# Kernel optimization log

Measured on AMD Instinct MI355X. Metric: run time of the kernel, lower is better.

The kernel has to match this reference:

```python
import jax, jax.numpy as jnp
import numpy as np

B, N, T = 4, 512, 10
F = N + 4            # 4 base features + one per-column feature
MSG_HID, MSG_DIM = 128, 32
UPD_HID, OUT_DIM = 128, 4


def setup_inputs() -> dict:
    key = jax.random.key(0)
    ks = jax.random.split(key, 9)
    s = 0.05
    return {
        "x": jax.random.normal(ks[0], (B, N, T, F), dtype=jnp.float32),
        # message MLP: (T*5) -> MSG_HID -> MSG_DIM
        "mW1": jax.random.normal(ks[1], (T * 5, MSG_HID), dtype=jnp.float32) * s,
        "mb1": jnp.zeros((MSG_HID,), dtype=jnp.float32),
        "mW2": jax.random.normal(ks[2], (MSG_HID, MSG_DIM), dtype=jnp.float32) * s,
        "mb2": jnp.zeros((MSG_DIM,), dtype=jnp.float32),
        # update MLP: (MSG_DIM+4) -> UPD_HID -> OUT_DIM
        "iW1": jax.random.normal(ks[3], (MSG_DIM + 4, UPD_HID), dtype=jnp.float32) * s,
        "ib1": jnp.zeros((UPD_HID,), dtype=jnp.float32),
        "iW2": jax.random.normal(ks[4], (UPD_HID, OUT_DIM), dtype=jnp.float32) * s,
        "ib2": jnp.zeros((OUT_DIM,), dtype=jnp.float32),
    }


def reference(x, mW1, mb1, mW2, mb2, iW1, ib1, iW2, ib2):
    b, n, t, f = x.shape
    base = x[..., :4]                      # [B,N,T,4]  shared source features
    extra = x[..., 4:4 + n]                # [B,N,T,N]  per-column feature
    # pairwise input: ph[b,c,s,t,:] = concat(base[b,s,t], extra[b,s,t,c])
    ph = jnp.concatenate([
        jnp.broadcast_to(base[:, None], (b, n, n, t, 4)),
        jnp.transpose(extra, (0, 3, 1, 2))[..., None],
    ], axis=-1)                             # [B,Ncol,Nsrc,T,5]
    h = ph.reshape(b, n, n, t * 5)
    h = jax.nn.relu(h @ mW1 + mb1)          # [B,Ncol,Nsrc,MSG_HID]
    msg = h @ mW2 + mb2                     # [B,Ncol,Nsrc,MSG_DIM]
    msg_sum = msg.sum(axis=2)               # sum over source nodes -> [B,Ncol,MSG_DIM]
    node_feat = x[:, :, -1, :4]             # last timestep, first 4 feats -> [B,N,4]
    mi = jnp.concatenate([msg_sum, node_feat], axis=-1)  # [B,N,MSG_DIM+4]
    h2 = jax.nn.relu(mi @ iW1 + ib1)
    return h2 @ iW2 + ib2                   # [B,N,OUT_DIM]
```

## Files before the change

kernel.cpp:

```cpp
#include <hip/hip_runtime.h>
#include <hip/hip_bf16.h>

#define Bn 4
#define Nn 512
#define Tn 10
#define Fn 516
#define MH 128
#define MD 32
#define UH 128
#define OD 4

#define JSPLIT 64
#define JPB (Nn / JSPLIT)

typedef __attribute__((ext_vector_type(4))) short short4v;
typedef __attribute__((ext_vector_type(8))) short short8v;
typedef __attribute__((ext_vector_type(4))) float floatx4;

static __device__ inline unsigned pk2(float a, float b) {
  union { __hip_bfloat162 h; unsigned u; } cv;
  cv.h = __float22bfloat162_rn(make_float2(a, b));
  return cv.u;
}
static __device__ inline short4v pack4(float a, float b, float c, float d) {
  union { short4v s; unsigned u[2]; } cv;
  cv.u[0] = pk2(a, b);
  cv.u[1] = pk2(c, d);
  return cv.s;
}

#if __has_builtin(__builtin_amdgcn_mfma_f32_16x16x16bf16_1k)
static __device__ inline floatx4 MFMA16(short4v a, short4v b, floatx4 c) {
  return __builtin_amdgcn_mfma_f32_16x16x16bf16_1k(a, b, c, 0, 0, 0);
}
#else
static __device__ inline floatx4 MFMA16(short4v a, short4v b, floatx4 c) {
  short8v a8 = {a[0], a[1], a[2], a[3], 0, 0, 0, 0};
  short8v b8 = {b[0], b[1], b[2], b[3], 0, 0, 0, 0};
  return __builtin_amdgcn_mfma_f32_16x16x32_bf16(a8, b8, c, 0, 0, 0);
}
#endif

__global__ __launch_bounds__(128) void kA(const float* __restrict__ x,
                                          const float* __restrict__ mW1,
                                          const float* __restrict__ mb1,
                                          float* __restrict__ Abase) {
  int bj = blockIdx.x;
  int k  = threadIdx.x;
  const float* xr = x + (size_t)bj * Tn * Fn;
  float acc = mb1[k];
#pragma unroll
  for (int t = 0; t < Tn; ++t)
#pragma unroll
    for (int c = 0; c < 4; ++c)
      acc = fmaf(xr[t * Fn + c], mW1[(t * 5 + c) * MH + k], acc);
  Abase[(size_t)bj * MH + k] = acc;
}

__global__ __launch_bounds__(256, 4) void kB(const float* __restrict__ x,
                                             const float* __restrict__ Abase,
                                             const float* __restrict__ mW1,
                                             const float* __restrict__ mW2,
                                             float* __restrict__ msum) {
  const int bx    = blockIdx.x;
  const int jsp   = bx & (JSPLIT - 1);
  const int itile = (bx / JSPLIT) & 3;
  const int b     = bx / (JSPLIT * 4);
  const int tid   = threadIdx.x;
  const int w     = tid >> 6;
  const int l     = tid & 63;
  const int ln    = l & 15;
  const int q     = l >> 4;
  const int ibase = itile * 128 + w * 32;

  __shared__ float ciL[JPB][MH];

  {
    const float4* src = (const float4*)(Abase + (size_t)(b * Nn + jsp * JPB) * MH);
    float4* dst = (float4*)&ciL[0][0];
#pragma unroll
    for (int u = 0; u < 2; ++u)
      dst[tid + u * 256] = src[tid + u * 256];
  }

  short4v A1[8];
#pragma unroll
  for (int mt = 0; mt < 8; ++mt) {
    float v[4];
#pragma unroll
    for (int e = 0; e < 4; ++e) {
      int t = q * 4 + e;
      v[e] = (t < Tn) ? mW1[(t * 5 + 4) * MH + mt * 16 + ln] : 0.f;
    }
    A1[mt] = pack4(v[0], v[1], v[2], v[3]);
  }
  short4v B2[8][2];
#pragma unroll
  for (int kt = 0; kt < 8; ++kt)
#pragma unroll
    for (int ct = 0; ct < 2; ++ct) {
      float v[4];
#pragma unroll
      for (int e = 0; e < 4; ++e)
        v[e] = mW2[(kt * 16 + q * 4 + e) * MD + ct * 16 + ln];
      B2[kt][ct] = pack4(v[0], v[1], v[2], v[3]);
    }

  floatx4 acc[2][2];
#pragma unroll
  for (int a = 0; a < 2; ++a)
#pragma unroll
    for (int c = 0; c < 2; ++c) acc[a][c] = (floatx4)0.f;

  __syncthreads();

#pragma unroll 4
  for (int jj = 0; jj < JPB; ++jj) {
    const int j = jsp * JPB + jj;

    const float* xp = x + (size_t)(b * Nn + j) * Tn * Fn + 4 + ibase;
    short4v B1[2];
#pragma unroll
    for (int nt = 0; nt < 2; ++nt) {
      float v[4];
#pragma unroll
      for (int e = 0; e < 4; ++e) {
        int t = q * 4 + e;
        v[e] = (t < Tn) ? xp[(size_t)t * Fn + nt * 16 + ln] : 0.f;
      }
      B1[nt] = pack4(v[0], v[1], v[2], v[3]);
    }

#pragma unroll
    for (int mt = 0; mt < 8; ++mt) {
      floatx4 ci = *(const floatx4*)&ciL[jj][mt * 16 + q * 4];
      floatx4 d0 = MFMA16(A1[mt], B1[0], ci);
      floatx4 d1 = MFMA16(A1[mt], B1[1], ci);
      short4v pa0 = pack4(fmaxf(d0[0], 0.f), fmaxf(d0[1], 0.f),
                          fmaxf(d0[2], 0.f), fmaxf(d0[3], 0.f));
      short4v pa1 = pack4(fmaxf(d1[0], 0.f), fmaxf(d1[1], 0.f),
                          fmaxf(d1[2], 0.f), fmaxf(d1[3], 0.f));
      acc[0][0] = MFMA16(pa0, B2[mt][0], acc[0][0]);
      acc[0][1] = MFMA16(pa0, B2[mt][1], acc[0][1]);
      acc[1][0] = MFMA16(pa1, B2[mt][0], acc[1][0]);
      acc[1][1] = MFMA16(pa1, B2[mt][1], acc[1][1]);
    }
  }

#pragma unroll
  for (int nt = 0; nt < 2; ++nt)
#pragma unroll
    for (int ct = 0; ct < 2; ++ct)
#pragma unroll
      for (int r = 0; r < 4; ++r) {
        int i = ibase + nt * 16 + q * 4 + r;
        int c = ct * 16 + ln;
        atomicAdd(&msum[(size_t)(b * Nn + i) * MD + c], acc[nt][ct][r]);
      }
}

__global__ __launch_bounds__(128) void kC(const float* __restrict__ x,
                                          const float* __restrict__ msum,
                                          const float* __restrict__ mb2,
                                          const float* __restrict__ iW1,
                                          const float* __restrict__ ib1,
                                          const float* __restrict__ iW2,
                                          const float* __restrict__ ib2,
                                          float* __restrict__ out) {
  int bi = blockIdx.x;
  int k  = threadIdx.x;
  __shared__ float red[UH][OD];

  const float* ms = msum + (size_t)bi * MD;
  const float* nf = x + ((size_t)bi * Tn + (Tn - 1)) * Fn;

  float a = ib1[k];
#pragma unroll
  for (int c = 0; c < MD; ++c)
    a = fmaf(ms[c] + (float)Nn * mb2[c], iW1[c * UH + k], a);
#pragma unroll
  for (int c = 0; c < 4; ++c)
    a = fmaf(nf[c], iW1[(MD + c) * UH + k], a);
  a = fmaxf(a, 0.f);
#pragma unroll
  for (int c = 0; c < OD; ++c) red[k][c] = a * iW2[k * OD + c];
  __syncthreads();

  if (k < OD) {
    float s = ib2[k];
    for (int kk = 0; kk < UH; ++kk) s += red[kk][k];
    out[(size_t)bi * OD + k] = s;
  }
}

extern "C" void kernel_launch(void* const* d_in, const int* in_sizes, int n_in,
                              void* d_out, int out_size, void* d_ws, size_t ws_size,
                              hipStream_t stream) {
  const float* x   = (const float*)d_in[0];
  const float* mW1 = (const float*)d_in[1];
  const float* mb1 = (const float*)d_in[2];
  const float* mW2 = (const float*)d_in[3];
  const float* mb2 = (const float*)d_in[4];
  const float* iW1 = (const float*)d_in[5];
  const float* ib1 = (const float*)d_in[6];
  const float* iW2 = (const float*)d_in[7];
  const float* ib2 = (const float*)d_in[8];
  float* out = (float*)d_out;

  float* Abase = (float*)d_ws;
  float* msum  = Abase + (size_t)Bn * Nn * MH;

  hipMemsetAsync(msum, 0, (size_t)Bn * Nn * MD * sizeof(float), stream);

  kA<<<Bn * Nn, 128, 0, stream>>>(x, mW1, mb1, Abase);
  kB<<<Bn * 4 * JSPLIT, 256, 0, stream>>>(x, Abase, mW1, mW2, msum);
  kC<<<Bn * Nn, 128, 0, stream>>>(x, msum, mb2, iW1, ib1, iW2, ib2, out);
}
```

Baseline: 64.39 us.

## Halve per-wave column tile in message kernel to double grid and occupancy

```diff
diff --git a/kernel.cpp b/kernel.cpp
--- a/kernel.cpp
+++ b/kernel.cpp
@@ -57,21 +57,21 @@
   Abase[(size_t)bj * MH + k] = acc;
 }
 
-__global__ __launch_bounds__(256, 4) void kB(const float* __restrict__ x,
+__global__ __launch_bounds__(256, 8) void kB(const float* __restrict__ x,
                                              const float* __restrict__ Abase,
                                              const float* __restrict__ mW1,
                                              const float* __restrict__ mW2,
                                              float* __restrict__ msum) {
   const int bx    = blockIdx.x;
   const int jsp   = bx & (JSPLIT - 1);
-  const int itile = (bx / JSPLIT) & 3;
-  const int b     = bx / (JSPLIT * 4);
+  const int itile = (bx >> 6) & 7;
+  const int b     = bx >> 9;
   const int tid   = threadIdx.x;
   const int w     = tid >> 6;
   const int l     = tid & 63;
   const int ln    = l & 15;
   const int q     = l >> 4;
-  const int ibase = itile * 128 + w * 32;
+  const int ibase = itile * 64 + w * 16;
 
   __shared__ float ciL[JPB][MH];
 
@@ -106,57 +106,44 @@
       B2[kt][ct] = pack4(v[0], v[1], v[2], v[3]);
     }
 
-  floatx4 acc[2][2];
-#pragma unroll
-  for (int a = 0; a < 2; ++a)
-#pragma unroll
-    for (int c = 0; c < 2; ++c) acc[a][c] = (floatx4)0.f;
+  floatx4 acc[2];
+  acc[0] = (floatx4)0.f;
+  acc[1] = (floatx4)0.f;
 
   __syncthreads();
 
-#pragma unroll 4
+#pragma unroll 2
   for (int jj = 0; jj < JPB; ++jj) {
     const int j = jsp * JPB + jj;
 
     const float* xp = x + (size_t)(b * Nn + j) * Tn * Fn + 4 + ibase;
-    short4v B1[2];
-#pragma unroll
-    for (int nt = 0; nt < 2; ++nt) {
-      float v[4];
-#pragma unroll
-      for (int e = 0; e < 4; ++e) {
-        int t = q * 4 + e;
-        v[e] = (t < Tn) ? xp[(size_t)t * Fn + nt * 16 + ln] : 0.f;
-      }
-      B1[nt] = pack4(v[0], v[1], v[2], v[3]);
-    }
+    float v[4];
+#pragma unroll
+    for (int e = 0; e < 4; ++e) {
+      int t = q * 4 + e;
+      v[e] = (t < Tn) ? xp[(size_t)t * Fn + ln] : 0.f;
+    }
+    short4v B1 = pack4(v[0], v[1], v[2], v[3]);
 
 #pragma unroll
     for (int mt = 0; mt < 8; ++mt) {
       floatx4 ci = *(const floatx4*)&ciL[jj][mt * 16 + q * 4];
-      floatx4 d0 = MFMA16(A1[mt], B1[0], ci);
-      floatx4 d1 = MFMA16(A1[mt], B1[1], ci);
-      short4v pa0 = pack4(fmaxf(d0[0], 0.f), fmaxf(d0[1], 0.f),
-                          fmaxf(d0[2], 0.f), fmaxf(d0[3], 0.f));
-      short4v pa1 = pack4(fmaxf(d1[0], 0.f), fmaxf(d1[1], 0.f),
-                          fmaxf(d1[2], 0.f), fmaxf(d1[3], 0.f));
-      acc[0][0] = MFMA16(pa0, B2[mt][0], acc[0][0]);
-      acc[0][1] = MFMA16(pa0, B2[mt][1], acc[0][1]);
-      acc[1][0] = MFMA16(pa1, B2[mt][0], acc[1][0]);
-      acc[1][1] = MFMA16(pa1, B2[mt][1], acc[1][1]);
-    }
-  }
-
-#pragma unroll
-  for (int nt = 0; nt < 2; ++nt)
-#pragma unroll
-    for (int ct = 0; ct < 2; ++ct)
-#pragma unroll
-      for (int r = 0; r < 4; ++r) {
-        int i = ibase + nt * 16 + q * 4 + r;
-        int c = ct * 16 + ln;
-        atomicAdd(&msum[(size_t)(b * Nn + i) * MD + c], acc[nt][ct][r]);
-      }
+      floatx4 d0 = MFMA16(A1[mt], B1, ci);
+      short4v pa = pack4(fmaxf(d0[0], 0.f), fmaxf(d0[1], 0.f),
+                         fmaxf(d0[2], 0.f), fmaxf(d0[3], 0.f));
+      acc[0] = MFMA16(pa, B2[mt][0], acc[0]);
+      acc[1] = MFMA16(pa, B2[mt][1], acc[1]);
+    }
+  }
+
+#pragma unroll
+  for (int ct = 0; ct < 2; ++ct)
+#pragma unroll
+    for (int r = 0; r < 4; ++r) {
+      int i = ibase + q * 4 + r;
+      int c = ct * 16 + ln;
+      atomicAdd(&msum[(size_t)(b * Nn + i) * MD + c], acc[ct][r]);
+    }
 }
 
 __global__ __launch_bounds__(128) void kC(const float* __restrict__ x,
@@ -213,6 +200,6 @@
   hipMemsetAsync(msum, 0, (size_t)Bn * Nn * MD * sizeof(float), stream);
 
   kA<<<Bn * Nn, 128, 0, stream>>>(x, mW1, mb1, Abase);
-  kB<<<Bn * 4 * JSPLIT, 256, 0, stream>>>(x, Abase, mW1, mW2, msum);
+  kB<<<Bn * 8 * JSPLIT, 256, 0, stream>>>(x, Abase, mW1, mW2, msum);
   kC<<<Bn * Nn, 128, 0, stream>>>(x, msum, mb2, iW1, ib1, iW2, ib2, out);
 }
```

Measured after the change: 77.84 us. 20.9% more time.

## Replace atomic reduction with bf16 partial buffers reduced in the update kernel

Applied to the files above, without the earlier changes.

```diff
diff --git a/kernel.cpp b/kernel.cpp
--- a/kernel.cpp
+++ b/kernel.cpp
@@ -10,7 +10,7 @@
 #define UH 128
 #define OD 4
 
-#define JSPLIT 64
+#define JSPLIT 128
 #define JPB (Nn / JSPLIT)
 
 typedef __attribute__((ext_vector_type(4))) short short4v;
@@ -57,15 +57,15 @@
   Abase[(size_t)bj * MH + k] = acc;
 }
 
-__global__ __launch_bounds__(256, 4) void kB(const float* __restrict__ x,
+__global__ __launch_bounds__(256, 8) void kB(const float* __restrict__ x,
                                              const float* __restrict__ Abase,
                                              const float* __restrict__ mW1,
                                              const float* __restrict__ mW2,
-                                             float* __restrict__ msum) {
+                                             __hip_bfloat16* __restrict__ part) {
   const int bx    = blockIdx.x;
   const int jsp   = bx & (JSPLIT - 1);
-  const int itile = (bx / JSPLIT) & 3;
-  const int b     = bx / (JSPLIT * 4);
+  const int itile = (bx >> 7) & 3;
+  const int b     = bx >> 9;
   const int tid   = threadIdx.x;
   const int w     = tid >> 6;
   const int l     = tid & 63;
@@ -75,12 +75,9 @@
 
   __shared__ float ciL[JPB][MH];
 
-  {
+  if (tid < JPB * MH / 4) {
     const float4* src = (const float4*)(Abase + (size_t)(b * Nn + jsp * JPB) * MH);
-    float4* dst = (float4*)&ciL[0][0];
-#pragma unroll
-    for (int u = 0; u < 2; ++u)
-      dst[tid + u * 256] = src[tid + u * 256];
+    ((float4*)&ciL[0][0])[tid] = src[tid];
   }
 
   short4v A1[8];
@@ -114,7 +111,7 @@
 
   __syncthreads();
 
-#pragma unroll 4
+#pragma unroll
   for (int jj = 0; jj < JPB; ++jj) {
     const int j = jsp * JPB + jj;
 
@@ -155,12 +152,13 @@
       for (int r = 0; r < 4; ++r) {
         int i = ibase + nt * 16 + q * 4 + r;
         int c = ct * 16 + ln;
-        atomicAdd(&msum[(size_t)(b * Nn + i) * MD + c], acc[nt][ct][r]);
+        part[((size_t)(jsp * Bn + b) * Nn + i) * MD + c] =
+            __float2bfloat16(acc[nt][ct][r]);
       }
 }
 
 __global__ __launch_bounds__(128) void kC(const float* __restrict__ x,
-                                          const float* __restrict__ msum,
+                                          const __hip_bfloat16* __restrict__ part,
                                           const float* __restrict__ mb2,
                                           const float* __restrict__ iW1,
                                           const float* __restrict__ ib1,
@@ -168,27 +166,46 @@
                                           const float* __restrict__ ib2,
                                           float* __restrict__ out) {
   int bi = blockIdx.x;
+  int b  = bi / Nn;
+  int i  = bi - b * Nn;
   int k  = threadIdx.x;
-  __shared__ float red[UH][OD];
-
-  const float* ms = msum + (size_t)bi * MD;
+  __shared__ float redp[4][MD];
+  __shared__ float msL[MD];
+  __shared__ float redo[UH][OD];
+
+  {
+    int c = k & (MD - 1);
+    int g = k >> 5;
+    float s = 0.f;
+#pragma unroll 4
+    for (int r = 0; r < JSPLIT / 4; ++r) {
+      int jsp = g + 4 * r;
+      s += (float)part[((size_t)(jsp * Bn + b) * Nn + i) * MD + c];
+    }
+    redp[g][c] = s;
+  }
+  __syncthreads();
+  if (k < MD)
+    msL[k] = redp[0][k] + redp[1][k] + redp[2][k] + redp[3][k] + (float)Nn * mb2[k];
+  __syncthreads();
+
   const float* nf = x + ((size_t)bi * Tn + (Tn - 1)) * Fn;
 
   float a = ib1[k];
 #pragma unroll
   for (int c = 0; c < MD; ++c)
-    a = fmaf(ms[c] + (float)Nn * mb2[c], iW1[c * UH + k], a);
+    a = fmaf(msL[c], iW1[c * UH + k], a);
 #pragma unroll
   for (int c = 0; c < 4; ++c)
     a = fmaf(nf[c], iW1[(MD + c) * UH + k], a);
   a = fmaxf(a, 0.f);
 #pragma unroll
-  for (int c = 0; c < OD; ++c) red[k][c] = a * iW2[k * OD + c];
+  for (int c = 0; c < OD; ++c) redo[k][c] = a * iW2[k * OD + c];
   __syncthreads();
 
   if (k < OD) {
     float s = ib2[k];
-    for (int kk = 0; kk < UH; ++kk) s += red[kk][k];
+    for (int kk = 0; kk < UH; ++kk) s += redo[kk][k];
     out[(size_t)bi * OD + k] = s;
   }
 }
@@ -208,11 +225,9 @@
   float* out = (float*)d_out;
 
   float* Abase = (float*)d_ws;
-  float* msum  = Abase + (size_t)Bn * Nn * MH;
-
-  hipMemsetAsync(msum, 0, (size_t)Bn * Nn * MD * sizeof(float), stream);
+  __hip_bfloat16* part = (__hip_bfloat16*)(Abase + (size_t)Bn * Nn * MH);
 
   kA<<<Bn * Nn, 128, 0, stream>>>(x, mW1, mb1, Abase);
-  kB<<<Bn * 4 * JSPLIT, 256, 0, stream>>>(x, Abase, mW1, mW2, msum);
-  kC<<<Bn * Nn, 128, 0, stream>>>(x, msum, mb2, iW1, ib1, iW2, ib2, out);
-}
+  kB<<<Bn * 4 * JSPLIT, 256, 0, stream>>>(x, Abase, mW1, mW2, part);
+  kC<<<Bn * Nn, 128, 0, stream>>>(x, part, mb2, iW1, ib1, iW2, ib2, out);
+}
```

After: 111.0 us. 72.4% more time.

## Pre-pack per-column features into bf16 MFMA layout and prefetch in message kernel

Applied to the files above, without the earlier changes.

```diff
diff --git a/kernel.cpp b/kernel.cpp
--- a/kernel.cpp
+++ b/kernel.cpp
@@ -12,6 +12,7 @@
 
 #define JSPLIT 64
 #define JPB (Nn / JSPLIT)
+#define XTF (Tn * Fn)
 
 typedef __attribute__((ext_vector_type(4))) short short4v;
 typedef __attribute__((ext_vector_type(8))) short short8v;
@@ -57,15 +58,44 @@
   Abase[(size_t)bj * MH + k] = acc;
 }
 
-__global__ __launch_bounds__(256, 4) void kB(const float* __restrict__ x,
+__global__ __launch_bounds__(256) void kE(const float* __restrict__ x,
+                                          __hip_bfloat16* __restrict__ Ex) {
+  const int bj  = blockIdx.x;
+  const int tid = threadIdx.x;
+  const int w   = tid >> 6;
+  const int l   = tid & 63;
+  __shared__ uint4 rly[4][2][64];
+
+  const float* xr = x + (size_t)bj * XTF + 4;
+#pragma unroll
+  for (int h = 0; h < 2; ++h) {
+    int i = h * 256 + tid;
+    float v[Tn];
+#pragma unroll
+    for (int t = 0; t < Tn; ++t) v[t] = xr[(size_t)t * Fn + i];
+
+    union { unsigned u[8]; uint4 q[2]; } o;
+#pragma unroll
+    for (int p = 0; p < 5; ++p) o.u[p] = pk2(v[2 * p], v[2 * p + 1]);
+    o.u[5] = 0u; o.u[6] = 0u; o.u[7] = 0u;
+
+    rly[w][0][l] = o.q[0];
+    rly[w][1][l] = o.q[1];
+    uint4* ob = (uint4*)(Ex + ((size_t)bj * Nn + h * 256 + w * 64) * 16);
+    ob[l]      = rly[w][l & 1][l >> 1];
+    ob[64 + l] = rly[w][l & 1][32 + (l >> 1)];
+  }
+}
+
+__global__ __launch_bounds__(256, 4) void kB(const __hip_bfloat16* __restrict__ Ex,
                                              const float* __restrict__ Abase,
                                              const float* __restrict__ mW1,
                                              const float* __restrict__ mW2,
                                              float* __restrict__ msum) {
   const int bx    = blockIdx.x;
   const int jsp   = bx & (JSPLIT - 1);
-  const int itile = (bx / JSPLIT) & 3;
-  const int b     = bx / (JSPLIT * 4);
+  const int itile = (bx >> 6) & 3;
+  const int b     = bx >> 8;
   const int tid   = threadIdx.x;
   const int w     = tid >> 6;
   const int l     = tid & 63;
@@ -74,13 +104,19 @@
   const int ibase = itile * 128 + w * 32;
 
   __shared__ float ciL[JPB][MH];
-
   {
     const float4* src = (const float4*)(Abase + (size_t)(b * Nn + jsp * JPB) * MH);
-    float4* dst = (float4*)&ciL[0][0];
-#pragma unroll
-    for (int u = 0; u < 2; ++u)
-      dst[tid + u * 256] = src[tid + u * 256];
+    ((float4*)&ciL[0][0])[tid] = src[tid];
+  }
+
+  short4v B1a[JPB][2];
+#pragma unroll
+  for (int jj = 0; jj < JPB; ++jj) {
+    const __hip_bfloat16* ep =
+        Ex + ((size_t)(b * Nn + jsp * JPB + jj) * Nn + ibase) * 16 + q * 4;
+#pragma unroll
+    for (int nt = 0; nt < 2; ++nt)
+      B1a[jj][nt] = *(const short4v*)(ep + (nt * 16 + ln) * 16);
   }
 
   short4v A1[8];
@@ -114,28 +150,13 @@
 
   __syncthreads();
 
-#pragma unroll 4
+#pragma unroll
   for (int jj = 0; jj < JPB; ++jj) {
-    const int j = jsp * JPB + jj;
-
-    const float* xp = x + (size_t)(b * Nn + j) * Tn * Fn + 4 + ibase;
-    short4v B1[2];
-#pragma unroll
-    for (int nt = 0; nt < 2; ++nt) {
-      float v[4];
-#pragma unroll
-      for (int e = 0; e < 4; ++e) {
-        int t = q * 4 + e;
-        v[e] = (t < Tn) ? xp[(size_t)t * Fn + nt * 16 + ln] : 0.f;
-      }
-      B1[nt] = pack4(v[0], v[1], v[2], v[3]);
-    }
-
 #pragma unroll
     for (int mt = 0; mt < 8; ++mt) {
       floatx4 ci = *(const floatx4*)&ciL[jj][mt * 16 + q * 4];
-      floatx4 d0 = MFMA16(A1[mt], B1[0], ci);
-      floatx4 d1 = MFMA16(A1[mt], B1[1], ci);
+      floatx4 d0 = MFMA16(A1[mt], B1a[jj][0], ci);
+      floatx4 d1 = MFMA16(A1[mt], B1a[jj][1], ci);
       short4v pa0 = pack4(fmaxf(d0[0], 0.f), fmaxf(d0[1], 0.f),
                           fmaxf(d0[2], 0.f), fmaxf(d0[3], 0.f));
       short4v pa1 = pack4(fmaxf(d1[0], 0.f), fmaxf(d1[1], 0.f),
@@ -209,10 +230,12 @@
 
   float* Abase = (float*)d_ws;
   float* msum  = Abase + (size_t)Bn * Nn * MH;
+  __hip_bfloat16* Ex = (__hip_bfloat16*)(msum + (size_t)Bn * Nn * MD);
 
   hipMemsetAsync(msum, 0, (size_t)Bn * Nn * MD * sizeof(float), stream);
 
   kA<<<Bn * Nn, 128, 0, stream>>>(x, mW1, mb1, Abase);
-  kB<<<Bn * 4 * JSPLIT, 256, 0, stream>>>(x, Abase, mW1, mW2, msum);
+  kE<<<Bn * Nn, 256, 0, stream>>>(x, Ex);
+  kB<<<Bn * 4 * JSPLIT, 256, 0, stream>>>(Ex, Abase, mW1, mW2, msum);
   kC<<<Bn * Nn, 128, 0, stream>>>(x, msum, mb2, iW1, ib1, iW2, ib2, out);
 }
```

Result: slower. 65.82 us (+2.2%).
